# Performance work log

Hardware: AMD Instinct MI355X
Metric: run time of the kernel (lower is better)

The kernel has to match this reference:

```python
import jax, jax.numpy as jnp
import numpy as np

N = 100000
E = 500000
D = 128      # input_dim
H = 4        # heads
C = 32       # per-head out channels (H*C == D)
HID = 512    # FFN hidden
EPS = 1e-5


def _layer_norm(x, w, b):
    mu = jnp.mean(x, axis=-1, keepdims=True)
    var = jnp.mean(jnp.square(x - mu), axis=-1, keepdims=True)
    return (x - mu) * jax.lax.rsqrt(var + EPS) * w + b


def setup_inputs() -> dict:
    key = jax.random.key(0)
    ks = jax.random.split(key, 16)
    s = 1.0 / np.sqrt(D)
    inp = {
        "x": jax.random.normal(ks[0], (N, D), dtype=jnp.float32),
        "edge_index": jax.random.randint(ks[1], (2, E), 0, N, dtype=jnp.int64),
        # TransformerConv params (lin_query/key/value/skip: D -> H*C == D)
        "Wq": jax.random.normal(ks[2], (D, D), dtype=jnp.float32) * s,
        "bq": jnp.zeros((D,), jnp.float32),
        "Wk": jax.random.normal(ks[3], (D, D), dtype=jnp.float32) * s,
        "bk": jnp.zeros((D,), jnp.float32),
        "Wv": jax.random.normal(ks[4], (D, D), dtype=jnp.float32) * s,
        "bv": jnp.zeros((D,), jnp.float32),
        "Wskip": jax.random.normal(ks[5], (D, D), dtype=jnp.float32) * s,
        "bskip": jnp.zeros((D,), jnp.float32),
        # lin_out
        "Wout": jax.random.normal(ks[6], (D, D), dtype=jnp.float32) * s,
        "bout": jnp.zeros((D,), jnp.float32),
        # LayerNorms
        "ln1_w": jnp.ones((D,), jnp.float32),
        "ln1_b": jnp.zeros((D,), jnp.float32),
        "ln2_w": jnp.ones((D,), jnp.float32),
        "ln2_b": jnp.zeros((D,), jnp.float32),
        # FFN
        "W1": jax.random.normal(ks[7], (HID, D), dtype=jnp.float32) * s,
        "b1": jnp.zeros((HID,), jnp.float32),
        "W2": jax.random.normal(ks[8], (D, HID), dtype=jnp.float32) * (1.0 / np.sqrt(HID)),
        "b2": jnp.zeros((D,), jnp.float32),
    }
    return inp


def _transformer_conv(x, src, dst, Wq, bq, Wk, bk, Wv, bv, Wskip, bskip):
    # q/k/v: [N, H, C]
    q = (x @ Wq.T + bq).reshape(N, H, C)
    k = (x @ Wk.T + bk).reshape(N, H, C)
    v = (x @ Wv.T + bv).reshape(N, H, C)
    # per-edge attention logits: [E, H]
    alpha = jnp.sum(q[dst] * k[src], axis=-1) / np.sqrt(C)
    # segment softmax over incoming edges of each destination node
    m = jax.ops.segment_max(alpha, dst, num_segments=N)       # [N, H]
    e = jnp.exp(alpha - m[dst])                               # [E, H]
    z = jax.ops.segment_sum(e, dst, num_segments=N)           # [N, H]
    a = e / z[dst]                                            # [E, H]
    # weighted aggregate of values: [N, H, C]
    msg = a[:, :, None] * v[src]
    out = jax.ops.segment_sum(msg, dst, num_segments=N)
    # root/skip connection (PyG root_weight=True)
    return out.reshape(N, H * C) + x @ Wskip.T + bskip


def reference(x, Wq, bq, Wk, bk, Wv, bv, Wskip, bskip, Wout, bout,
              ln1_w, ln1_b, W1, b1, W2, b2, ln2_w, ln2_b, edge_index):
    src = edge_index[0]
    dst = edge_index[1]
    conv = _transformer_conv(x, src, dst, Wq, bq, Wk, bk, Wv, bv, Wskip, bskip)
    out1 = conv @ Wout.T + bout
    out2 = _layer_norm(out1 + x, ln1_w, ln1_b)
    h = jax.nn.relu(out2 @ W1.T + b1)
    out3 = h @ W2.T + b2
    out4 = _layer_norm(out3 + out2, ln2_w, ln2_b)
    return out4
```

## Files before the change

kernel.cpp:

```cpp
#include <hip/hip_runtime.h>

#define NN   100000
#define NE   500000
#define DD   128
#define HH   4
#define HIDD 512
#define EPSF 1e-5f

typedef __bf16 bf16x8 __attribute__((ext_vector_type(8)));
typedef float  f32x4  __attribute__((ext_vector_type(4)));
typedef unsigned short u16x8 __attribute__((ext_vector_type(8)));

__device__ __forceinline__ unsigned short f2b(float f) {
  unsigned u = __float_as_uint(f);
  unsigned r = (u + 0x7FFFu + ((u >> 16) & 1)) >> 16;
  return (unsigned short)r;
}
__device__ __forceinline__ float b2f(unsigned short s) {
  return __uint_as_float(((unsigned)s) << 16);
}

#define GLOAD16(ldsp, gp) __builtin_amdgcn_global_load_lds(                      \
    (const __attribute__((address_space(1))) void*)(gp),                         \
    (__attribute__((address_space(3))) void*)(ldsp), 16, 0, 0)

template <int NT>
__device__ __forceinline__ void stage_tile(unsigned short* lds, const unsigned short* g,
                                           int ldg, int t) {
  const int w = t >> 6, l = t & 63;
#pragma unroll
  for (int i = 0; i < 2048 / NT; i++) {
    const int chunk0 = i * NT + w * 64;
    const int chunk = chunk0 + l;
    const int row = chunk >> 4, c16 = chunk & 15;
    const int gslot = c16 ^ (row & 15);
    GLOAD16(lds + (size_t)chunk0 * 8, g + (size_t)row * ldg + gslot * 8);
  }
}

__global__ void k_castw(const float* __restrict__ Wq, const float* __restrict__ Wk,
                        const float* __restrict__ Wv, const float* __restrict__ Wsk,
                        const float* __restrict__ Wo, const float* __restrict__ W1,
                        const float* __restrict__ W2,
                        const float* __restrict__ bq, const float* __restrict__ bk,
                        const float* __restrict__ bv, const float* __restrict__ bs,
                        unsigned short* __restrict__ Wqkvs, unsigned short* __restrict__ Wob,
                        unsigned short* __restrict__ W1b, unsigned short* __restrict__ W2b,
                        float* __restrict__ bias512) {
  int i = blockIdx.x * 256 + threadIdx.x;
  if (i < 53248) {
    int e = i * 4;
    const float* src; unsigned short* dst; int off;
    if (e < 65536) {
      int seg = e >> 14;
      const float* s4[4] = {Wq, Wk, Wv, Wsk};
      src = s4[seg]; dst = Wqkvs + (seg << 14); off = e & 16383;
    } else if (e < 81920) { src = Wo;  dst = Wob; off = e - 65536; }
    else if (e < 147456)  { src = W1;  dst = W1b; off = e - 81920; }
    else                  { src = W2;  dst = W2b; off = e - 147456; }
    float4 v = *(const float4*)&src[off];
    ushort4 o; o.x = f2b(v.x); o.y = f2b(v.y); o.z = f2b(v.z); o.w = f2b(v.w);
    *(ushort4*)&dst[off] = o;
  } else if (i < 53376) {
    int b4 = (i - 53248) * 4;
    const float* srcs[4] = {bq, bk, bv, bs};
#pragma unroll
    for (int j = 0; j < 4; j++) {
      int idx = b4 + j;
      bias512[idx] = srcs[idx >> 7][idx & 127];
    }
  }
}

__global__ void k_zero_cnt(int* __restrict__ cnt) {
  int i = blockIdx.x * 256 + threadIdx.x;
  if (i < NN) cnt[i] = 0;
}
__global__ void k_count(const int* __restrict__ ei, int* __restrict__ cnt) {
  int e = blockIdx.x * 256 + threadIdx.x;
  if (e < NE) atomicAdd(&cnt[ei[NE + e]], 1);
}
__global__ void k_scan1(const int* __restrict__ cnt, int* __restrict__ rowptr, int* __restrict__ part) {
  __shared__ int sh[256];
  int i = blockIdx.x * 256 + threadIdx.x;
  int v = (i < NN) ? cnt[i] : 0;
  sh[threadIdx.x] = v; __syncthreads();
  for (int off = 1; off < 256; off <<= 1) {
    int t = (threadIdx.x >= off) ? sh[threadIdx.x - off] : 0;
    __syncthreads();
    sh[threadIdx.x] += t;
    __syncthreads();
  }
  if (i < NN) rowptr[i] = sh[threadIdx.x] - v;
  if (threadIdx.x == 255) part[blockIdx.x] = sh[255];
}
__global__ void k_scan2(const int* __restrict__ part, int* __restrict__ partx) {
  __shared__ int sh[512];
  int t = threadIdx.x;
  int v = (t < 391) ? part[t] : 0;
  sh[t] = v; __syncthreads();
  for (int off = 1; off < 512; off <<= 1) {
    int u = (t >= off) ? sh[t - off] : 0;
    __syncthreads();
    sh[t] += u;
    __syncthreads();
  }
  partx[t] = sh[t] - v;
}
__global__ void k_scan3(int* __restrict__ rowptr, const int* __restrict__ partx, int* __restrict__ cnt) {
  int i = blockIdx.x * 256 + threadIdx.x;
  if (i < NN) {
    int r = rowptr[i] + partx[i >> 8];
    rowptr[i] = r;
    cnt[i] = r;
  }
  if (i == 0) rowptr[NN] = NE;
}
__global__ void k_scatter(const int* __restrict__ ei, int* __restrict__ cnt, int* __restrict__ csr_src) {
  int e = blockIdx.x * 256 + threadIdx.x;
  if (e >= NE) return;
  int d = ei[NE + e];
  int pos = atomicAdd(&cnt[d], 1);
  csr_src[pos] = ei[e];
}

#define LOADA(dst, Aptr, LDA_)                                                   \
  _Pragma("unroll") for (int ks = 0; ks < 4; ks++)                               \
    _Pragma("unroll") for (int rt = 0; rt < 2; rt++) {                           \
      const int row_ = n0 + rt * 16 + lq;                                        \
      bf16x8 zz = {};                                                            \
      dst[ks][rt] = (row_ < NN)                                                  \
          ? *(const bf16x8*)&(Aptr)[(size_t)row_ * (LDA_) + ks * 32 + hq * 8]    \
          : zz;                                                                  \
    }

#define LOADA_F32(dst, Xp)                                                       \
  _Pragma("unroll") for (int ks = 0; ks < 4; ks++)                               \
    _Pragma("unroll") for (int rt = 0; rt < 2; rt++) {                           \
      const int row_ = n0 + rt * 16 + lq;                                        \
      u16x8 tmp = {};                                                            \
      if (row_ < NN) {                                                           \
        const float* p = (Xp) + (size_t)row_ * 128 + ks * 32 + hq * 8;           \
        float4 f0 = *(const float4*)p, f1 = *(const float4*)(p + 4);             \
        tmp[0]=f2b(f0.x); tmp[1]=f2b(f0.y); tmp[2]=f2b(f0.z); tmp[3]=f2b(f0.w);  \
        tmp[4]=f2b(f1.x); tmp[5]=f2b(f1.y); tmp[6]=f2b(f1.z); tmp[7]=f2b(f1.w);  \
      }                                                                          \
      dst[ks][rt] = *(bf16x8*)&tmp;                                              \
    }

#define MFMA_PHASE(WS, AF, ACC)                                                  \
  _Pragma("unroll") for (int ks = 0; ks < 4; ks++) {                             \
    bf16x8 bb[8];                                                                \
    const int c16_ = ks * 4 + hq;                                                \
    _Pragma("unroll") for (int ct = 0; ct < 8; ct++) {                           \
      const int row_ = ct * 16 + lq;                                             \
      bb[ct] = *(const bf16x8*)&WS[row_ * 128 + ((c16_ ^ lq) * 8)];              \
    }                                                                            \
    _Pragma("unroll") for (int rt = 0; rt < 2; rt++)                             \
      _Pragma("unroll") for (int ct = 0; ct < 8; ct++)                           \
        ACC[rt][ct] = __builtin_amdgcn_mfma_f32_16x16x32_bf16(bb[ct], AF[ks][rt], ACC[rt][ct], 0, 0, 0); \
  }

__global__ __launch_bounds__(512, 2) void k_qkvs(const float* __restrict__ x,
                                                 const unsigned short* __restrict__ W,
                                                 const float* __restrict__ bias,
                                                 unsigned short* __restrict__ outB) {
  __shared__ __align__(16) unsigned short WsA[128 * 128];
  __shared__ __align__(16) unsigned short WsB[128 * 128];
  const int t = threadIdx.x;
  const int w = t >> 6, l = t & 63;
  const int n0 = blockIdx.x * 256 + w * 32;
  const int lq = l & 15, hq = l >> 4;

  bf16x8 af[4][2];
  LOADA_F32(af, x);
  stage_tile<512>(WsA, W, 128, t);
  __syncthreads();
#pragma unroll
  for (int cg = 0; cg < 4; ++cg) {
    unsigned short* cur = (cg & 1) ? WsB : WsA;
    unsigned short* nxt = (cg & 1) ? WsA : WsB;
    if (cg < 3) stage_tile<512>(nxt, W + (size_t)(cg + 1) * 128 * 128, 128, t);
    f32x4 acc[2][8] = {};
    MFMA_PHASE(cur, af, acc)
#pragma unroll
    for (int rt = 0; rt < 2; rt++) {
      const int row = n0 + rt * 16 + lq;
      if (row < NN) {
#pragma unroll
        for (int ct = 0; ct < 8; ct++) {
          const int col = cg * 128 + ct * 16 + hq * 4;
          const float4 bs = *(const float4*)&bias[col];
          ushort4 o;
          o.x = f2b(acc[rt][ct][0] + bs.x);
          o.y = f2b(acc[rt][ct][1] + bs.y);
          o.z = f2b(acc[rt][ct][2] + bs.z);
          o.w = f2b(acc[rt][ct][3] + bs.w);
          *(ushort4*)&outB[(size_t)row * 512 + col] = o;
        }
      }
    }
    if (cg < 3) __syncthreads();
  }
}

__global__ __launch_bounds__(512, 2) void k_post(const unsigned short* __restrict__ conv,
                                                 const float* __restrict__ x,
                                                 const unsigned short* __restrict__ Wob,
                                                 const float* __restrict__ bo,
                                                 const float* __restrict__ l1w,
                                                 const float* __restrict__ l1b,
                                                 const unsigned short* __restrict__ W1b,
                                                 const float* __restrict__ b1,
                                                 const unsigned short* __restrict__ W2b,
                                                 const float* __restrict__ b2,
                                                 const float* __restrict__ l2w,
                                                 const float* __restrict__ l2b,
                                                 float* __restrict__ outF) {
  __shared__ __align__(16) unsigned short WsA[128 * 128];
  __shared__ __align__(16) unsigned short WsB[128 * 128];
  __shared__ __align__(16) unsigned short Hs[256 * 128];
  const int t = threadIdx.x;
  const int w = t >> 6, l = t & 63;
  const int n0 = blockIdx.x * 256 + w * 32;
  const int lq = l & 15, hq = l >> 4;
  const int lrow = w * 32;

  bf16x8 af[4][2];
  LOADA(af, conv, 512);
  stage_tile<512>(WsA, Wob, 128, t);
  __syncthreads();
  stage_tile<512>(WsB, W1b, 128, t);

  f32x4 acc[2][8] = {};
  MFMA_PHASE(WsA, af, acc)

  ushort4 o2[2][8];
#pragma unroll
  for (int rt = 0; rt < 2; rt++) {
    const int row = n0 + rt * 16 + lq;
#pragma unroll
    for (int ct = 0; ct < 8; ct++) {
      const int col = ct * 16 + hq * 4;
      const float4 bs = *(const float4*)&bo[col];
      float4 rv = make_float4(0.f, 0.f, 0.f, 0.f);
      if (row < NN) rv = *(const float4*)&x[(size_t)row * DD + col];
      acc[rt][ct][0] += bs.x + rv.x;
      acc[rt][ct][1] += bs.y + rv.y;
      acc[rt][ct][2] += bs.z + rv.z;
      acc[rt][ct][3] += bs.w + rv.w;
    }
    float s = 0.f;
#pragma unroll
    for (int ct = 0; ct < 8; ct++)
#pragma unroll
      for (int j = 0; j < 4; j++) s += acc[rt][ct][j];
    s += __shfl_xor(s, 16, 64); s += __shfl_xor(s, 32, 64);
    const float mu = s * (1.f / 128.f);
    float vs = 0.f;
#pragma unroll
    for (int ct = 0; ct < 8; ct++)
#pragma unroll
      for (int j = 0; j < 4; j++) { float d = acc[rt][ct][j] - mu; vs += d * d; }
    vs += __shfl_xor(vs, 16, 64); vs += __shfl_xor(vs, 32, 64);
    const float rs = rsqrtf(vs * (1.f / 128.f) + EPSF);
    const int hrow = lrow + rt * 16 + lq;
#pragma unroll
    for (int ct = 0; ct < 8; ct++) {
      const int col = ct * 16 + hq * 4;
      const float4 lw4 = *(const float4*)&l1w[col];
      const float4 lb4 = *(const float4*)&l1b[col];
      ushort4 o;
      o.x = f2b((acc[rt][ct][0] - mu) * rs * lw4.x + lb4.x);
      o.y = f2b((acc[rt][ct][1] - mu) * rs * lw4.y + lb4.y);
      o.z = f2b((acc[rt][ct][2] - mu) * rs * lw4.z + lb4.z);
      o.w = f2b((acc[rt][ct][3] - mu) * rs * lw4.w + lb4.w);
      o2[rt][ct] = o;
      *(ushort4*)&Hs[hrow * 128 + (((col >> 3) ^ lq) * 8) + (col & 7)] = o;
    }
  }
  __syncthreads();

  bf16x8 af2[4][2];
#pragma unroll
  for (int ks = 0; ks < 4; ks++)
#pragma unroll
    for (int rt = 0; rt < 2; rt++)
      af2[ks][rt] = *(const bf16x8*)&Hs[(lrow + rt * 16 + lq) * 128 + (((ks * 4 + hq) ^ lq) * 8)];

  f32x4 acc2[2][8] = {};
#pragma unroll 1
  for (int cg = 0; cg < 4; ++cg) {
    stage_tile<512>(WsA, W2b + (size_t)cg * 128, 512, t);
    f32x4 acc1[2][8] = {};
    MFMA_PHASE(WsB, af2, acc1)
#pragma unroll
    for (int rt = 0; rt < 2; rt++) {
      const int hrow = lrow + rt * 16 + lq;
#pragma unroll
      for (int ct = 0; ct < 8; ct++) {
        const int col = ct * 16 + hq * 4;
        const float4 bs = *(const float4*)&b1[cg * 128 + col];
        ushort4 o;
        o.x = f2b(fmaxf(acc1[rt][ct][0] + bs.x, 0.f));
        o.y = f2b(fmaxf(acc1[rt][ct][1] + bs.y, 0.f));
        o.z = f2b(fmaxf(acc1[rt][ct][2] + bs.z, 0.f));
        o.w = f2b(fmaxf(acc1[rt][ct][3] + bs.w, 0.f));
        *(ushort4*)&Hs[hrow * 128 + (((col >> 3) ^ lq) * 8) + (col & 7)] = o;
      }
    }
    __syncthreads();
    if (cg < 3) stage_tile<512>(WsB, W1b + (size_t)(cg + 1) * 128 * 128, 128, t);
#pragma unroll
    for (int ks = 0; ks < 4; ks++) {
      bf16x8 bb[8];
      const int c16_ = ks * 4 + hq;
#pragma unroll
      for (int ct = 0; ct < 8; ct++) {
        const int row_ = ct * 16 + lq;
        bb[ct] = *(const bf16x8*)&WsA[row_ * 128 + ((c16_ ^ lq) * 8)];
      }
      bf16x8 h[2];
#pragma unroll
      for (int rt = 0; rt < 2; rt++)
        h[rt] = *(const bf16x8*)&Hs[(lrow + rt * 16 + lq) * 128 + ((c16_ ^ lq) * 8)];
#pragma unroll
      for (int rt = 0; rt < 2; rt++)
#pragma unroll
        for (int ct = 0; ct < 8; ct++)
          acc2[rt][ct] = __builtin_amdgcn_mfma_f32_16x16x32_bf16(bb[ct], h[rt], acc2[rt][ct], 0, 0, 0);
    }
    __syncthreads();
  }

#pragma unroll
  for (int rt = 0; rt < 2; rt++) {
    const int row = n0 + rt * 16 + lq;
#pragma unroll
    for (int ct = 0; ct < 8; ct++) {
      const int col = ct * 16 + hq * 4;
      const float4 bs = *(const float4*)&b2[col];
      const ushort4 rv = o2[rt][ct];
      acc2[rt][ct][0] += bs.x + b2f(rv.x);
      acc2[rt][ct][1] += bs.y + b2f(rv.y);
      acc2[rt][ct][2] += bs.z + b2f(rv.z);
      acc2[rt][ct][3] += bs.w + b2f(rv.w);
    }
    float s = 0.f;
#pragma unroll
    for (int ct = 0; ct < 8; ct++)
#pragma unroll
      for (int j = 0; j < 4; j++) s += acc2[rt][ct][j];
    s += __shfl_xor(s, 16, 64); s += __shfl_xor(s, 32, 64);
    const float mu = s * (1.f / 128.f);
    float vs = 0.f;
#pragma unroll
    for (int ct = 0; ct < 8; ct++)
#pragma unroll
      for (int j = 0; j < 4; j++) { float d = acc2[rt][ct][j] - mu; vs += d * d; }
    vs += __shfl_xor(vs, 16, 64); vs += __shfl_xor(vs, 32, 64);
    const float rs = rsqrtf(vs * (1.f / 128.f) + EPSF);
    if (row < NN) {
#pragma unroll
      for (int ct = 0; ct < 8; ct++) {
        const int col = ct * 16 + hq * 4;
        const float4 lw4 = *(const float4*)&l2w[col];
        const float4 lb4 = *(const float4*)&l2b[col];
        float4 o;
        o.x = (acc2[rt][ct][0] - mu) * rs * lw4.x + lb4.x;
        o.y = (acc2[rt][ct][1] - mu) * rs * lw4.y + lb4.y;
        o.z = (acc2[rt][ct][2] - mu) * rs * lw4.z + lb4.z;
        o.w = (acc2[rt][ct][3] - mu) * rs * lw4.w + lb4.w;
        *(float4*)&outF[(size_t)row * DD + col] = o;
      }
    }
  }
}

__global__ __launch_bounds__(256) void k_attn(const int* __restrict__ csr_src,
                                              const int* __restrict__ rowptr,
                                              unsigned short* qkvsb) {
  const int l = threadIdx.x & 31;
  const int node = blockIdx.x * 8 + (threadIdx.x >> 5);
  const int row0 = rowptr[node], row1 = rowptr[node + 1];
  ushort4 qu = *(const ushort4*)&qkvsb[(size_t)node * 512 + l * 4];
  const float qx = b2f(qu.x), qy = b2f(qu.y), qz = b2f(qu.z), qw = b2f(qu.w);
  float ax = 0.f, ay = 0.f, az = 0.f, aw = 0.f, z = 0.f;
  int p = row0;
  for (; p + 2 <= row1; p += 2) {
    int s0 = csr_src[p], s1 = csr_src[p + 1];
    const unsigned short* b0 = &qkvsb[(size_t)s0 * 512];
    const unsigned short* b1 = &qkvsb[(size_t)s1 * 512];
    ushort4 k0 = *(const ushort4*)(b0 + 128 + l * 4);
    ushort4 v0 = *(const ushort4*)(b0 + 256 + l * 4);
    ushort4 k1 = *(const ushort4*)(b1 + 128 + l * 4);
    ushort4 v1 = *(const ushort4*)(b1 + 256 + l * 4);
    float d0 = qx * b2f(k0.x) + qy * b2f(k0.y) + qz * b2f(k0.z) + qw * b2f(k0.w);
    float d1 = qx * b2f(k1.x) + qy * b2f(k1.y) + qz * b2f(k1.z) + qw * b2f(k1.w);
    d0 += __shfl_xor(d0, 1, 32); d1 += __shfl_xor(d1, 1, 32);
    d0 += __shfl_xor(d0, 2, 32); d1 += __shfl_xor(d1, 2, 32);
    d0 += __shfl_xor(d0, 4, 32); d1 += __shfl_xor(d1, 4, 32);
    float e0 = __expf(d0 * 0.17677669529663687f);
    float e1 = __expf(d1 * 0.17677669529663687f);
    z += e0 + e1;
    ax += e0 * b2f(v0.x) + e1 * b2f(v1.x);
    ay += e0 * b2f(v0.y) + e1 * b2f(v1.y);
    az += e0 * b2f(v0.z) + e1 * b2f(v1.z);
    aw += e0 * b2f(v0.w) + e1 * b2f(v1.w);
  }
  if (p < row1) {
    int s = csr_src[p];
    const unsigned short* base = &qkvsb[(size_t)s * 512];
    ushort4 kr = *(const ushort4*)(base + 128 + l * 4);
    ushort4 vr = *(const ushort4*)(base + 256 + l * 4);
    float d = qx * b2f(kr.x) + qy * b2f(kr.y) + qz * b2f(kr.z) + qw * b2f(kr.w);
    d += __shfl_xor(d, 1, 32);
    d += __shfl_xor(d, 2, 32);
    d += __shfl_xor(d, 4, 32);
    float e = __expf(d * 0.17677669529663687f);
    z += e;
    ax += e * b2f(vr.x); ay += e * b2f(vr.y);
    az += e * b2f(vr.z); aw += e * b2f(vr.w);
  }
  const float rz = (z > 0.f) ? (1.f / z) : 0.f;
  ushort4 su = *(const ushort4*)&qkvsb[(size_t)node * 512 + 384 + l * 4];
  ushort4 o;
  o.x = f2b(b2f(su.x) + ax * rz);
  o.y = f2b(b2f(su.y) + ay * rz);
  o.z = f2b(b2f(su.z) + az * rz);
  o.w = f2b(b2f(su.w) + aw * rz);
  *(ushort4*)&qkvsb[(size_t)node * 512 + 384 + l * 4] = o;
}

extern "C" void kernel_launch(void* const* d_in, const int* in_sizes, int n_in,
                              void* d_out, int out_size, void* d_ws, size_t ws_size,
                              hipStream_t stream) {
  const float* x   = (const float*)d_in[0];
  const int*   ei  = (const int*)d_in[1];
  const float* Wq  = (const float*)d_in[2];
  const float* bq  = (const float*)d_in[3];
  const float* Wk  = (const float*)d_in[4];
  const float* bk  = (const float*)d_in[5];
  const float* Wv  = (const float*)d_in[6];
  const float* bv  = (const float*)d_in[7];
  const float* Wsk = (const float*)d_in[8];
  const float* bsk = (const float*)d_in[9];
  const float* Wo  = (const float*)d_in[10];
  const float* bo  = (const float*)d_in[11];
  const float* l1w = (const float*)d_in[12];
  const float* l1b = (const float*)d_in[13];
  const float* l2w = (const float*)d_in[14];
  const float* l2b = (const float*)d_in[15];
  const float* W1  = (const float*)d_in[16];
  const float* b1  = (const float*)d_in[17];
  const float* W2  = (const float*)d_in[18];
  const float* b2  = (const float*)d_in[19];

  unsigned short* wsu = (unsigned short*)d_ws;
  unsigned short* qkvsb = wsu;
  int* csr_src = (int*)(qkvsb + (size_t)NN * 512);
  int* rowptr  = csr_src + NE;
  int* cnt     = rowptr + NN + 1;
  int* part    = cnt + NN;
  int* partx   = part + 512;
  size_t woff = (size_t)((partx + 512) - (int*)d_ws);
  woff = (woff + 3) & ~(size_t)3;
  unsigned short* Wqkvs = (unsigned short*)((int*)d_ws + woff);
  unsigned short* Wob   = Wqkvs + 512 * DD;
  unsigned short* W1b   = Wob + DD * DD;
  unsigned short* W2b   = W1b + (size_t)HIDD * DD;
  float* bias512        = (float*)(W2b + (size_t)DD * HIDD);

  float* outf = (float*)d_out;

  const int GB = (NN + 255) / 256;
  dim3 blk(256), blk5(512);

  k_castw<<<dim3(209), blk, 0, stream>>>(Wq, Wk, Wv, Wsk, Wo, W1, W2, bq, bk, bv, bsk,
                                         Wqkvs, Wob, W1b, W2b, bias512);

  k_zero_cnt<<<dim3(391), blk, 0, stream>>>(cnt);
  k_count<<<dim3(1954), blk, 0, stream>>>(ei, cnt);
  k_scan1<<<dim3(391), blk, 0, stream>>>(cnt, rowptr, part);
  k_scan2<<<dim3(1), dim3(512), 0, stream>>>(part, partx);
  k_scan3<<<dim3(391), blk, 0, stream>>>(rowptr, partx, cnt);
  k_scatter<<<dim3(1954), blk, 0, stream>>>(ei, cnt, csr_src);

  k_qkvs<<<dim3(GB), blk5, 0, stream>>>(x, Wqkvs, bias512, qkvsb);

  k_attn<<<dim3(12500), blk, 0, stream>>>(csr_src, rowptr, qkvsb);

  k_post<<<dim3(GB), blk5, 0, stream>>>(qkvsb + 384, x, Wob, bo, l1w, l1b,
                                        W1b, b1, W2b, b2, l2w, l2b, outf);
}
```

Before: 275.3 us.

## Split post-attention kernel into out-proj+LN1 and fused FFN+LN2 kernels

Splits the monolithic k_post kernel (512 threads, 256 rows, three 32KB-or-larger LDS buffers) into two kernels with 256 threads and 128 rows per block. The first computes out-projection and LN1 and writes a bf16 intermediate to global memory. The second runs the FFN with a single shared weight buffer reloaded for W1 and W2 in each chunk, which lowers LDS use and may raise occupancy but adds a global round-trip and extra barriers. The attention kernel's edge loop is also unrolled from 2 to 4 to put more gathers in flight.

```diff
diff --git a/kernel.cpp b/kernel.cpp
--- a/kernel.cpp
+++ b/kernel.cpp
@@ -204,45 +204,32 @@
   }
 }
 
-__global__ __launch_bounds__(512, 2) void k_post(const unsigned short* __restrict__ conv,
-                                                 const float* __restrict__ x,
-                                                 const unsigned short* __restrict__ Wob,
-                                                 const float* __restrict__ bo,
-                                                 const float* __restrict__ l1w,
-                                                 const float* __restrict__ l1b,
-                                                 const unsigned short* __restrict__ W1b,
-                                                 const float* __restrict__ b1,
-                                                 const unsigned short* __restrict__ W2b,
-                                                 const float* __restrict__ b2,
-                                                 const float* __restrict__ l2w,
-                                                 const float* __restrict__ l2b,
-                                                 float* __restrict__ outF) {
-  __shared__ __align__(16) unsigned short WsA[128 * 128];
-  __shared__ __align__(16) unsigned short WsB[128 * 128];
-  __shared__ __align__(16) unsigned short Hs[256 * 128];
+__global__ __launch_bounds__(256, 4) void k_gemm_ln1(const unsigned short* __restrict__ A,
+                                                     const float* __restrict__ x,
+                                                     const unsigned short* __restrict__ W,
+                                                     const float* __restrict__ bias,
+                                                     const float* __restrict__ lw,
+                                                     const float* __restrict__ lb,
+                                                     unsigned short* __restrict__ outB) {
+  __shared__ __align__(16) unsigned short Ws[128 * 128];
   const int t = threadIdx.x;
   const int w = t >> 6, l = t & 63;
-  const int n0 = blockIdx.x * 256 + w * 32;
+  const int n0 = blockIdx.x * 128 + w * 32;
   const int lq = l & 15, hq = l >> 4;
-  const int lrow = w * 32;
 
   bf16x8 af[4][2];
-  LOADA(af, conv, 512);
-  stage_tile<512>(WsA, Wob, 128, t);
+  LOADA(af, A, 512);
+  stage_tile<256>(Ws, W, 128, t);
   __syncthreads();
-  stage_tile<512>(WsB, W1b, 128, t);
-
   f32x4 acc[2][8] = {};
-  MFMA_PHASE(WsA, af, acc)
-
-  ushort4 o2[2][8];
+  MFMA_PHASE(Ws, af, acc)
 #pragma unroll
   for (int rt = 0; rt < 2; rt++) {
     const int row = n0 + rt * 16 + lq;
 #pragma unroll
     for (int ct = 0; ct < 8; ct++) {
       const int col = ct * 16 + hq * 4;
-      const float4 bs = *(const float4*)&bo[col];
+      const float4 bs = *(const float4*)&bias[col];
       float4 rv = make_float4(0.f, 0.f, 0.f, 0.f);
       if (row < NN) rv = *(const float4*)&x[(size_t)row * DD + col];
       acc[rt][ct][0] += bs.x + rv.x;
@@ -264,39 +251,53 @@
       for (int j = 0; j < 4; j++) { float d = acc[rt][ct][j] - mu; vs += d * d; }
     vs += __shfl_xor(vs, 16, 64); vs += __shfl_xor(vs, 32, 64);
     const float rs = rsqrtf(vs * (1.f / 128.f) + EPSF);
-    const int hrow = lrow + rt * 16 + lq;
-#pragma unroll
-    for (int ct = 0; ct < 8; ct++) {
-      const int col = ct * 16 + hq * 4;
-      const float4 lw4 = *(const float4*)&l1w[col];
-      const float4 lb4 = *(const float4*)&l1b[col];
-      ushort4 o;
-      o.x = f2b((acc[rt][ct][0] - mu) * rs * lw4.x + lb4.x);
-      o.y = f2b((acc[rt][ct][1] - mu) * rs * lw4.y + lb4.y);
-      o.z = f2b((acc[rt][ct][2] - mu) * rs * lw4.z + lb4.z);
-      o.w = f2b((acc[rt][ct][3] - mu) * rs * lw4.w + lb4.w);
-      o2[rt][ct] = o;
-      *(ushort4*)&Hs[hrow * 128 + (((col >> 3) ^ lq) * 8) + (col & 7)] = o;
-    }
-  }
-  __syncthreads();
-
-  bf16x8 af2[4][2];
-#pragma unroll
-  for (int ks = 0; ks < 4; ks++)
-#pragma unroll
-    for (int rt = 0; rt < 2; rt++)
-      af2[ks][rt] = *(const bf16x8*)&Hs[(lrow + rt * 16 + lq) * 128 + (((ks * 4 + hq) ^ lq) * 8)];
+    if (row < NN) {
+#pragma unroll
+      for (int ct = 0; ct < 8; ct++) {
+        const int col = ct * 16 + hq * 4;
+        const float4 lw4 = *(const float4*)&lw[col];
+        const float4 lb4 = *(const float4*)&lb[col];
+        ushort4 o;
+        o.x = f2b((acc[rt][ct][0] - mu) * rs * lw4.x + lb4.x);
+        o.y = f2b((acc[rt][ct][1] - mu) * rs * lw4.y + lb4.y);
+        o.z = f2b((acc[rt][ct][2] - mu) * rs * lw4.z + lb4.z);
+        o.w = f2b((acc[rt][ct][3] - mu) * rs * lw4.w + lb4.w);
+        *(ushort4*)&outB[(size_t)row * DD + col] = o;
+      }
+    }
+  }
+}
+
+__global__ __launch_bounds__(256, 1) void k_ffn_fused(const unsigned short* __restrict__ A,
+                                                      const unsigned short* __restrict__ W1,
+                                                      const float* __restrict__ b1,
+                                                      const unsigned short* __restrict__ W2,
+                                                      const float* __restrict__ b2,
+                                                      const float* __restrict__ lw,
+                                                      const float* __restrict__ lb,
+                                                      float* __restrict__ outF) {
+  __shared__ __align__(16) unsigned short Ws[128 * 128];
+  __shared__ __align__(16) unsigned short Hs[128 * 128];
+  const int t = threadIdx.x;
+  const int w = t >> 6, l = t & 63;
+  const int n0 = blockIdx.x * 128 + w * 32;
+  const int lq = l & 15, hq = l >> 4;
+  const int lrow = w * 32;
+
+  bf16x8 af[4][2];
+  LOADA(af, A, 128);
 
   f32x4 acc2[2][8] = {};
 #pragma unroll 1
   for (int cg = 0; cg < 4; ++cg) {
-    stage_tile<512>(WsA, W2b + (size_t)cg * 128, 512, t);
+    if (cg) __syncthreads();
+    stage_tile<256>(Ws, W1 + (size_t)cg * 128 * 128, 128, t);
+    __syncthreads();
     f32x4 acc1[2][8] = {};
-    MFMA_PHASE(WsB, af2, acc1)
+    MFMA_PHASE(Ws, af, acc1)
 #pragma unroll
     for (int rt = 0; rt < 2; rt++) {
-      const int hrow = lrow + rt * 16 + lq;
+      const int row = lrow + rt * 16 + lq;
 #pragma unroll
       for (int ct = 0; ct < 8; ct++) {
         const int col = ct * 16 + hq * 4;
@@ -306,11 +307,12 @@
         o.y = f2b(fmaxf(acc1[rt][ct][1] + bs.y, 0.f));
         o.z = f2b(fmaxf(acc1[rt][ct][2] + bs.z, 0.f));
         o.w = f2b(fmaxf(acc1[rt][ct][3] + bs.w, 0.f));
-        *(ushort4*)&Hs[hrow * 128 + (((col >> 3) ^ lq) * 8) + (col & 7)] = o;
+        *(ushort4*)&Hs[row * 128 + (((col >> 3) ^ lq) * 8) + (col & 7)] = o;
       }
     }
     __syncthreads();
-    if (cg < 3) stage_tile<512>(WsB, W1b + (size_t)(cg + 1) * 128 * 128, 128, t);
+    stage_tile<256>(Ws, W2 + (size_t)cg * 128, 512, t);
+    __syncthreads();
 #pragma unroll
     for (int ks = 0; ks < 4; ks++) {
       bf16x8 bb[8];
@@ -318,7 +320,7 @@
 #pragma unroll
       for (int ct = 0; ct < 8; ct++) {
         const int row_ = ct * 16 + lq;
-        bb[ct] = *(const bf16x8*)&WsA[row_ * 128 + ((c16_ ^ lq) * 8)];
+        bb[ct] = *(const bf16x8*)&Ws[row_ * 128 + ((c16_ ^ lq) * 8)];
       }
       bf16x8 h[2];
 #pragma unroll
@@ -330,7 +332,6 @@
         for (int ct = 0; ct < 8; ct++)
           acc2[rt][ct] = __builtin_amdgcn_mfma_f32_16x16x32_bf16(bb[ct], h[rt], acc2[rt][ct], 0, 0, 0);
     }
-    __syncthreads();
   }
 
 #pragma unroll
@@ -340,7 +341,8 @@
     for (int ct = 0; ct < 8; ct++) {
       const int col = ct * 16 + hq * 4;
       const float4 bs = *(const float4*)&b2[col];
-      const ushort4 rv = o2[rt][ct];
+      ushort4 rv = make_ushort4(0, 0, 0, 0);
+      if (row < NN) rv = *(const ushort4*)&A[(size_t)row * DD + col];
       acc2[rt][ct][0] += bs.x + b2f(rv.x);
       acc2[rt][ct][1] += bs.y + b2f(rv.y);
       acc2[rt][ct][2] += bs.z + b2f(rv.z);
@@ -364,8 +366,8 @@
 #pragma unroll
       for (int ct = 0; ct < 8; ct++) {
         const int col = ct * 16 + hq * 4;
-        const float4 lw4 = *(const float4*)&l2w[col];
-        const float4 lb4 = *(const float4*)&l2b[col];
+        const float4 lw4 = *(const float4*)&lw[col];
+        const float4 lb4 = *(const float4*)&lb[col];
         float4 o;
         o.x = (acc2[rt][ct][0] - mu) * rs * lw4.x + lb4.x;
         o.y = (acc2[rt][ct][1] - mu) * rs * lw4.y + lb4.y;
@@ -387,32 +389,41 @@
   const float qx = b2f(qu.x), qy = b2f(qu.y), qz = b2f(qu.z), qw = b2f(qu.w);
   float ax = 0.f, ay = 0.f, az = 0.f, aw = 0.f, z = 0.f;
   int p = row0;
-  for (; p + 2 <= row1; p += 2) {
-    int s0 = csr_src[p], s1 = csr_src[p + 1];
-    const unsigned short* b0 = &qkvsb[(size_t)s0 * 512];
-    const unsigned short* b1 = &qkvsb[(size_t)s1 * 512];
-    ushort4 k0 = *(const ushort4*)(b0 + 128 + l * 4);
-    ushort4 v0 = *(const ushort4*)(b0 + 256 + l * 4);
-    ushort4 k1 = *(const ushort4*)(b1 + 128 + l * 4);
-    ushort4 v1 = *(const ushort4*)(b1 + 256 + l * 4);
+  for (; p + 4 <= row1; p += 4) {
+    int s0 = csr_src[p], s1 = csr_src[p + 1], s2 = csr_src[p + 2], s3 = csr_src[p + 3];
+    const unsigned short* g0 = &qkvsb[(size_t)s0 * 512 + l * 4];
+    const unsigned short* g1 = &qkvsb[(size_t)s1 * 512 + l * 4];
+    const unsigned short* g2 = &qkvsb[(size_t)s2 * 512 + l * 4];
+    const unsigned short* g3 = &qkvsb[(size_t)s3 * 512 + l * 4];
+    ushort4 k0 = *(const ushort4*)(g0 + 128), v0 = *(const ushort4*)(g0 + 256);
+    ushort4 k1 = *(const ushort4*)(g1 + 128), v1 = *(const ushort4*)(g1 + 256);
+    ushort4 k2 = *(const ushort4*)(g2 + 128), v2 = *(const ushort4*)(g2 + 256);
+    ushort4 k3 = *(const ushort4*)(g3 + 128), v3 = *(const ushort4*)(g3 + 256);
     float d0 = qx * b2f(k0.x) + qy * b2f(k0.y) + qz * b2f(k0.z) + qw * b2f(k0.w);
     float d1 = qx * b2f(k1.x) + qy * b2f(k1.y) + qz * b2f(k1.z) + qw * b2f(k1.w);
+    float d2 = qx * b2f(k2.x) + qy * b2f(k2.y) + qz * b2f(k2.z) + qw * b2f(k2.w);
+    float d3 = qx * b2f(k3.x) + qy * b2f(k3.y) + qz * b2f(k3.z) + qw * b2f(k3.w);
     d0 += __shfl_xor(d0, 1, 32); d1 += __shfl_xor(d1, 1, 32);
+    d2 += __shfl_xor(d2, 1, 32); d3 += __shfl_xor(d3, 1, 32);
     d0 += __shfl_xor(d0, 2, 32); d1 += __shfl_xor(d1, 2, 32);
+    d2 += __shfl_xor(d2, 2, 32); d3 += __shfl_xor(d3, 2, 32);
     d0 += __shfl_xor(d0, 4, 32); d1 += __shfl_xor(d1, 4, 32);
+    d2 += __shfl_xor(d2, 4, 32); d3 += __shfl_xor(d3, 4, 32);
     float e0 = __expf(d0 * 0.17677669529663687f);
     float e1 = __expf(d1 * 0.17677669529663687f);
-    z += e0 + e1;
-    ax += e0 * b2f(v0.x) + e1 * b2f(v1.x);
-    ay += e0 * b2f(v0.y) + e1 * b2f(v1.y);
-    az += e0 * b2f(v0.z) + e1 * b2f(v1.z);
-    aw += e0 * b2f(v0.w) + e1 * b2f(v1.w);
-  }
-  if (p < row1) {
+    float e2 = __expf(d2 * 0.17677669529663687f);
+    float e3 = __expf(d3 * 0.17677669529663687f);
+    z += (e0 + e1) + (e2 + e3);
+    ax += e0 * b2f(v0.x) + e1 * b2f(v1.x) + e2 * b2f(v2.x) + e3 * b2f(v3.x);
+    ay += e0 * b2f(v0.y) + e1 * b2f(v1.y) + e2 * b2f(v2.y) + e3 * b2f(v3.y);
+    az += e0 * b2f(v0.z) + e1 * b2f(v1.z) + e2 * b2f(v2.z) + e3 * b2f(v3.z);
+    aw += e0 * b2f(v0.w) + e1 * b2f(v1.w) + e2 * b2f(v2.w) + e3 * b2f(v3.w);
+  }
+  for (; p < row1; ++p) {
     int s = csr_src[p];
-    const unsigned short* base = &qkvsb[(size_t)s * 512];
-    ushort4 kr = *(const ushort4*)(base + 128 + l * 4);
-    ushort4 vr = *(const ushort4*)(base + 256 + l * 4);
+    const unsigned short* base = &qkvsb[(size_t)s * 512 + l * 4];
+    ushort4 kr = *(const ushort4*)(base + 128);
+    ushort4 vr = *(const ushort4*)(base + 256);
     float d = qx * b2f(kr.x) + qy * b2f(kr.y) + qz * b2f(kr.z) + qw * b2f(kr.w);
     d += __shfl_xor(d, 1, 32);
     d += __shfl_xor(d, 2, 32);
@@ -458,7 +469,8 @@
 
   unsigned short* wsu = (unsigned short*)d_ws;
   unsigned short* qkvsb = wsu;
-  int* csr_src = (int*)(qkvsb + (size_t)NN * 512);
+  unsigned short* out2b = wsu + (size_t)NN * 512;
+  int* csr_src = (int*)(out2b + (size_t)NN * DD);
   int* rowptr  = csr_src + NE;
   int* cnt     = rowptr + NN + 1;
   int* part    = cnt + NN;
@@ -473,6 +485,7 @@
 
   float* outf = (float*)d_out;
 
+  const int GX = (NN + 127) / 128;
   const int GB = (NN + 255) / 256;
   dim3 blk(256), blk5(512);
 
@@ -490,6 +503,7 @@
 
   k_attn<<<dim3(12500), blk, 0, stream>>>(csr_src, rowptr, qkvsb);
 
-  k_post<<<dim3(GB), blk5, 0, stream>>>(qkvsb + 384, x, Wob, bo, l1w, l1b,
-                                        W1b, b1, W2b, b2, l2w, l2b, outf);
-}
+  k_gemm_ln1<<<dim3(GX), blk, 0, stream>>>(qkvsb + 384, x, Wob, bo, l1w, l1b, out2b);
+
+  k_ffn_fused<<<dim3(GX), blk, 0, stream>>>(out2b, W1b, b1, W2b, b2, l2w, l2b, outf);
+}
```

After: 306.2 us. 1.11x slower.
